# Optimization experiments

Hardware: AMD Instinct MI355X
Metric: run time of the kernel (lower is better)

Reference implementation:

```python
import jax, jax.numpy as jnp
import numpy as np

B = 16777216

def setup_inputs() -> dict:
    key = jax.random.key(0)
    k1, k2 = jax.random.split(key)
    x = jax.random.normal(k1, (B, 2), dtype=jnp.float32)
    ws = jax.random.normal(k2, (10,), dtype=jnp.float32)  # 10 scalar Linear(1,1) weights
    return {"x": x, "ws": ws}

def _step(carry, w):
    x0, x1 = carry
    nx0 = x0 - 0.1 * x1
    nx1 = 0.1 * x0 + x1 - 0.1 * x0**3 + 0.1 * (w * x1)
    return (nx0, nx1), None

def reference(x, ws):
    (x0, x1), _ = jax.lax.scan(_step, (x[:, 0], x[:, 1]), ws)
    out = (jnp.tanh(100.0 * (x1 - 0.1)) - jnp.tanh(100.0 * (x1 + 0.1)) + 2.0) / 2.0
    return out[:, None]  # [B, 1]
```

## Files before the change

### kernel.cpp

```cpp
#include <hip/hip_runtime.h>

typedef float v2f __attribute__((ext_vector_type(2)));

__device__ __forceinline__ v2f pk_fma(v2f a, v2f b, v2f c) {
    v2f d;
    asm("v_pk_fma_f32 %0, %1, %2, %3" : "=v"(d) : "v"(a), "v"(b), "v"(c));
    return d;
}
__device__ __forceinline__ v2f pk_mul(v2f a, v2f b) {
    v2f d;
    asm("v_pk_mul_f32 %0, %1, %2" : "=v"(d) : "v"(a), "v"(b));
    return d;
}

__device__ __forceinline__ float band(float x1) {
    float E  = __builtin_amdgcn_exp2f(fmaf(288.539008f, x1, 28.8539008f));
    float Eu = E * 4.248354255291589e-18f;
    return 1.0f + __builtin_amdgcn_rcpf(E + 1.0f) - __builtin_amdgcn_rcpf(Eu + 1.0f);
}

__global__ void __launch_bounds__(256)
dynsys_kernel(const float4* __restrict__ x, const float* __restrict__ ws,
              v2f* __restrict__ out, int T) {
    int i = blockIdx.x * 256 + threadIdx.x;
    if (i >= T) return;

    v2f wn[10];
#pragma unroll
    for (int k = 0; k < 10; ++k) { float v = -ws[k]; wn[k] = (v2f){v, v}; }
    const v2f mone = {-1.0f, -1.0f};
    const v2f cn01 = {-0.1f, -0.1f};

    float4 ld[8];
#pragma unroll
    for (int k = 0; k < 8; ++k) ld[k] = x[i + k * T];

#pragma unroll
    for (int k = 0; k < 8; ++k) {
        v2f a0 = {ld[k].x, ld[k].z};
        v2f a1 = {ld[k].y, ld[k].w};
#pragma unroll
        for (int s = 0; s < 10; ++s) {
            v2f na0 = pk_fma(cn01, a1, a0);
            v2f t   = pk_fma(a0, a0, mone);
            v2f u   = pk_mul(a0, t);
            v2f d   = pk_fma(wn[s], a1, u);
            a1      = pk_fma(cn01, d, a1);
            a0      = na0;
        }
        v2f r = {band(a1.x), band(a1.y)};
        __builtin_nontemporal_store(r, &out[i + k * T]);
    }
}

extern "C" void kernel_launch(void* const* d_in, const int* in_sizes, int n_in,
                              void* d_out, int out_size, void* d_ws, size_t ws_size,
                              hipStream_t stream) {
    const float4* x  = (const float4*)d_in[0];
    const float*  ws = (const float*)d_in[1];
    v2f* out = (v2f*)d_out;

    int n4 = in_sizes[0] / 4;
    int T  = n4 / 8;
    int blocks = (T + 255) / 256;
    dynsys_kernel<<<blocks, 256, 0, stream>>>(x, ws, out, T);
}
```

Baseline: 214.0 us.

## Use two float4 rows per thread, interleaved recurrences, and a symmetric band formula

Each thread now handles 2 float4 loads instead of 8, giving 4x more threads and blocks, and the two independent recurrence chains are interleaved for ILP. The band function is rewritten using |x1| symmetry so it needs one exp2 and one rcp instead of one exp2 and two rcp. The bounds check is removed and the grid assumes T is a multiple of 256, which holds only for the fixed input size. The aim is more memory-level parallelism through higher occupancy and less transcendental work, at the cost of more per-thread setup overhead from loading ws.

```diff
diff --git a/kernel.cpp b/kernel.cpp
--- a/kernel.cpp
+++ b/kernel.cpp
@@ -14,16 +14,18 @@
 }
 
 __device__ __forceinline__ float band(float x1) {
-    float E  = __builtin_amdgcn_exp2f(fmaf(288.539008f, x1, 28.8539008f));
-    float Eu = E * 4.248354255291589e-18f;
-    return 1.0f + __builtin_amdgcn_rcpf(E + 1.0f) - __builtin_amdgcn_rcpf(Eu + 1.0f);
+    const float S = 2.4258257e8f;
+    const float K = 2.4258257e8f;
+    float t = __builtin_fabsf(x1);
+    float F = __builtin_amdgcn_exp2f(288.53900817779268f * t);
+    float r = __builtin_amdgcn_rcpf(fmaf(0.5f, F, K));
+    return fmaf(-S, r, 1.0f);
 }
 
 __global__ void __launch_bounds__(256)
 dynsys_kernel(const float4* __restrict__ x, const float* __restrict__ ws,
               v2f* __restrict__ out, int T) {
     int i = blockIdx.x * 256 + threadIdx.x;
-    if (i >= T) return;
 
     v2f wn[10];
 #pragma unroll
@@ -31,26 +33,33 @@
     const v2f mone = {-1.0f, -1.0f};
     const v2f cn01 = {-0.1f, -0.1f};
 
-    float4 ld[8];
-#pragma unroll
-    for (int k = 0; k < 8; ++k) ld[k] = x[i + k * T];
+    float4 va = x[i];
+    float4 vb = x[i + T];
+
+    v2f a0 = {va.x, va.z}, a1 = {va.y, va.w};
+    v2f b0 = {vb.x, vb.z}, b1 = {vb.y, vb.w};
 
 #pragma unroll
-    for (int k = 0; k < 8; ++k) {
-        v2f a0 = {ld[k].x, ld[k].z};
-        v2f a1 = {ld[k].y, ld[k].w};
-#pragma unroll
-        for (int s = 0; s < 10; ++s) {
-            v2f na0 = pk_fma(cn01, a1, a0);
-            v2f t   = pk_fma(a0, a0, mone);
-            v2f u   = pk_mul(a0, t);
-            v2f d   = pk_fma(wn[s], a1, u);
-            a1      = pk_fma(cn01, d, a1);
-            a0      = na0;
-        }
-        v2f r = {band(a1.x), band(a1.y)};
-        __builtin_nontemporal_store(r, &out[i + k * T]);
+    for (int s = 0; s < 10; ++s) {
+        v2f na0 = pk_fma(cn01, a1, a0);
+        v2f ta  = pk_fma(a0, a0, mone);
+        v2f ua  = pk_mul(a0, ta);
+        v2f da  = pk_fma(wn[s], a1, ua);
+        a1      = pk_fma(cn01, da, a1);
+        a0      = na0;
+
+        v2f nb0 = pk_fma(cn01, b1, b0);
+        v2f tb  = pk_fma(b0, b0, mone);
+        v2f ub  = pk_mul(b0, tb);
+        v2f db  = pk_fma(wn[s], b1, ub);
+        b1      = pk_fma(cn01, db, b1);
+        b0      = nb0;
     }
+
+    v2f ra = {band(a1.x), band(a1.y)};
+    v2f rb = {band(b1.x), band(b1.y)};
+    __builtin_nontemporal_store(ra, &out[i]);
+    __builtin_nontemporal_store(rb, &out[i + T]);
 }
 
 extern "C" void kernel_launch(void* const* d_in, const int* in_sizes, int n_in,
@@ -61,7 +70,7 @@
     v2f* out = (v2f*)d_out;
 
     int n4 = in_sizes[0] / 4;
-    int T  = n4 / 8;
-    int blocks = (T + 255) / 256;
+    int T  = n4 / 2;
+    int blocks = T / 256;
     dynsys_kernel<<<blocks, 256, 0, stream>>>(x, ws, out, T);
 }
```

Result: faster. 208.6 us (-2.5%).

## Use symmetric single-exp band formula and a grid-stride persistent loop

Applied to the files above, without the earlier changes.

The output band function is rewritten to use the symmetry in |x1|. It now needs one exp2 and one reciprocal per element instead of one exp2 and two reciprocals. The launch changes from one block per tile to a fixed 2048-block grid-stride loop, and input loads become nontemporal. Together these aim to cut transcendental work, reduce block scheduling overhead and lower cache pollution. The loop has no tail bounds check, so it assumes the element count divides evenly by the per-iteration stride.

```diff
diff --git a/kernel.cpp b/kernel.cpp
--- a/kernel.cpp
+++ b/kernel.cpp
@@ -1,6 +1,7 @@
 #include <hip/hip_runtime.h>
 
 typedef float v2f __attribute__((ext_vector_type(2)));
+typedef float v4f __attribute__((ext_vector_type(4)));
 
 __device__ __forceinline__ v2f pk_fma(v2f a, v2f b, v2f c) {
     v2f d;
@@ -14,16 +15,19 @@
 }
 
 __device__ __forceinline__ float band(float x1) {
-    float E  = __builtin_amdgcn_exp2f(fmaf(288.539008f, x1, 28.8539008f));
-    float Eu = E * 4.248354255291589e-18f;
-    return 1.0f + __builtin_amdgcn_rcpf(E + 1.0f) - __builtin_amdgcn_rcpf(Eu + 1.0f);
+    const float S = 2.4258257e8f;
+    float t = __builtin_fabsf(x1);
+    float F = __builtin_amdgcn_exp2f(288.53900817779268f * t);
+    float r = __builtin_amdgcn_rcpf(fmaf(0.5f, F, S));
+    return fmaf(-S, r, 1.0f);
 }
 
 __global__ void __launch_bounds__(256)
-dynsys_kernel(const float4* __restrict__ x, const float* __restrict__ ws,
-              v2f* __restrict__ out, int T) {
-    int i = blockIdx.x * 256 + threadIdx.x;
-    if (i >= T) return;
+dynsys_kernel(const v4f* __restrict__ x, const float* __restrict__ ws,
+              v2f* __restrict__ out, int n4) {
+    const int tid    = blockIdx.x * 256 + threadIdx.x;
+    const int nthr   = gridDim.x * 256;
+    const int per_it = nthr * 8;
 
     v2f wn[10];
 #pragma unroll
@@ -31,37 +35,38 @@
     const v2f mone = {-1.0f, -1.0f};
     const v2f cn01 = {-0.1f, -0.1f};
 
-    float4 ld[8];
+    for (int base = tid; base < n4; base += per_it) {
+        v4f ld[8];
 #pragma unroll
-    for (int k = 0; k < 8; ++k) ld[k] = x[i + k * T];
+        for (int k = 0; k < 8; ++k)
+            ld[k] = __builtin_nontemporal_load(&x[base + k * nthr]);
 
 #pragma unroll
-    for (int k = 0; k < 8; ++k) {
-        v2f a0 = {ld[k].x, ld[k].z};
-        v2f a1 = {ld[k].y, ld[k].w};
+        for (int k = 0; k < 8; ++k) {
+            v2f a0 = {ld[k].x, ld[k].z};
+            v2f a1 = {ld[k].y, ld[k].w};
 #pragma unroll
-        for (int s = 0; s < 10; ++s) {
-            v2f na0 = pk_fma(cn01, a1, a0);
-            v2f t   = pk_fma(a0, a0, mone);
-            v2f u   = pk_mul(a0, t);
-            v2f d   = pk_fma(wn[s], a1, u);
-            a1      = pk_fma(cn01, d, a1);
-            a0      = na0;
+            for (int s = 0; s < 10; ++s) {
+                v2f na0 = pk_fma(cn01, a1, a0);
+                v2f t   = pk_fma(a0, a0, mone);
+                v2f u   = pk_mul(a0, t);
+                v2f d   = pk_fma(wn[s], a1, u);
+                a1      = pk_fma(cn01, d, a1);
+                a0      = na0;
+            }
+            v2f r = {band(a1.x), band(a1.y)};
+            __builtin_nontemporal_store(r, &out[base + k * nthr]);
         }
-        v2f r = {band(a1.x), band(a1.y)};
-        __builtin_nontemporal_store(r, &out[i + k * T]);
     }
 }
 
 extern "C" void kernel_launch(void* const* d_in, const int* in_sizes, int n_in,
                               void* d_out, int out_size, void* d_ws, size_t ws_size,
                               hipStream_t stream) {
-    const float4* x  = (const float4*)d_in[0];
-    const float*  ws = (const float*)d_in[1];
+    const v4f*  x  = (const v4f*)d_in[0];
+    const float* ws = (const float*)d_in[1];
     v2f* out = (v2f*)d_out;
 
     int n4 = in_sizes[0] / 4;
-    int T  = n4 / 8;
-    int blocks = (T + 255) / 256;
-    dynsys_kernel<<<blocks, 256, 0, stream>>>(x, ws, out, T);
+    dynsys_kernel<<<2048, 256, 0, stream>>>(x, ws, out, n4);
 }
```

Measured after the change: 204.0 us. -4.7%, faster.
